# Optimization experiments

Hardware: AMD Instinct MI355X
Metric: run time of the kernel (lower is better)

## Reference

```python
import jax, jax.numpy as jnp
import numpy as np

B, S, D = 2, 2048, 1024
H, HD = 16, 64          # num_heads, head_dim
K = 32                  # JL n_components


def setup_inputs() -> dict:
    key = jax.random.key(0)
    k1, k2, k3, k4 = jax.random.split(key, 4)
    return {
        "hidden_states": jax.random.normal(k1, (B, S, D), dtype=jnp.float32),
        "W_attn": jax.random.normal(k2, (D, 3 * D), dtype=jnp.float32) * 0.02,
        "b_attn": jnp.zeros((3 * D,), dtype=jnp.float32),
        "S_proj": jax.random.normal(k3, (K, HD), dtype=jnp.float32) / np.sqrt(K),
        "W_proj": jax.random.normal(k4, (D, D), dtype=jnp.float32) * 0.02,
        "b_proj": jnp.zeros((D,), dtype=jnp.float32),
    }


def reference(hidden_states, W_attn, b_attn, S_proj, W_proj, b_proj):
    b, s, d = hidden_states.shape
    # GPT2 Conv1D: x @ W + b, then split into q,k,v
    qkv = hidden_states @ W_attn + b_attn            # [B,S,3D]
    q, k, v = jnp.split(qkv, 3, axis=-1)
    # split heads -> [B,H,S,HD]
    def split_heads(x):
        return x.reshape(b, s, H, HD).transpose(0, 2, 1, 3)
    q = split_heads(q) @ S_proj.T                    # [B,H,S,K] JL-reduced
    k = split_heads(k) @ S_proj.T                    # [B,H,S,K]
    v = split_heads(v)                               # [B,H,S,HD]
    # naive attention: scale by sqrt(value head_dim) per GPT2 _attn
    scores = jnp.einsum("bhqk,bhsk->bhqs", q, k) / jnp.sqrt(
        jnp.asarray(HD, dtype=v.dtype))              # [B,H,S,S]
    causal = jnp.tril(jnp.ones((s, s), dtype=bool))
    mask_value = jnp.finfo(scores.dtype).min
    scores = jnp.where(causal, scores, mask_value)
    attn = jax.nn.softmax(scores, axis=-1)
    out = jnp.einsum("bhqs,bhsd->bhqd", attn, v)     # [B,H,S,HD]
    out = out.transpose(0, 2, 1, 3).reshape(b, s, d)  # merge heads
    return out @ W_proj + b_proj
```

## Files before the change

kernel.cpp:

```cpp
#include <hip/hip_runtime.h>
#include <hip/hip_bf16.h>
#include <stdint.h>

#define B_ 2
#define S_ 2048
#define D_ 1024
#define H_ 16
#define HD_ 64
#define KJL 32
#define N3 3072

typedef __attribute__((ext_vector_type(8))) __bf16 bf16x8;
typedef __attribute__((ext_vector_type(4))) float floatx4;
typedef __attribute__((ext_vector_type(4))) short short4v;
typedef __attribute__((ext_vector_type(2))) unsigned int uint2v;

__device__ __forceinline__ unsigned short f2b(float x) {
  union { float f; unsigned u; } v; v.f = x;
  unsigned r = v.u + 0x7fffu + ((v.u >> 16) & 1u);
  return (unsigned short)(r >> 16);
}

__device__ __forceinline__ unsigned int pkbf(float lo, float hi) {
  union { float f; unsigned u; } a, b;
  a.f = lo; b.f = hi;
  return __builtin_amdgcn_perm(b.u + 0x8000u, a.u + 0x8000u, 0x07060302u);
}

__device__ __forceinline__ void async16(const void* g, void* l) {
  __builtin_amdgcn_global_load_lds((__attribute__((address_space(1))) void*)(g),
                                   (__attribute__((address_space(3))) void*)(l),
                                   16, 0, 0);
}

__global__ void cvt_kernel(const float* __restrict__ in,
                           unsigned short* __restrict__ out, int n) {
  int i = blockIdx.x * blockDim.x + threadIdx.x;
  int stride = gridDim.x * blockDim.x;
  for (; i < n; i += stride) out[i] = f2b(in[i]);
}

__global__ void tcvt_kernel(const float* __restrict__ in,
                            unsigned short* __restrict__ out, int R, int C) {
  __shared__ float t[32][33];
  int c0 = blockIdx.x * 32, r0 = blockIdx.y * 32;
  int tx = threadIdx.x, ty = threadIdx.y;
  for (int j = 0; j < 32; j += 8)
    t[ty + j][tx] = in[(r0 + ty + j) * C + c0 + tx];
  __syncthreads();
  for (int j = 0; j < 32; j += 8)
    out[(c0 + ty + j) * R + r0 + tx] = f2b(t[tx][ty + j]);
}

__global__ __launch_bounds__(256, 2)
void qkv_gemm_kernel(const unsigned short* __restrict__ A,
                     const unsigned short* __restrict__ Bt,
                     const float* __restrict__ bias,
                     unsigned short* __restrict__ Qh,
                     unsigned short* __restrict__ Kh,
                     unsigned short* __restrict__ Vc) {
  __shared__ __align__(16) unsigned short As[128 * 32];
  __shared__ __align__(16) unsigned short Bs[128 * 32];
  const int tid = threadIdx.x;
  const int lane = tid & 63, wv = tid >> 6;
  const int quad = lane >> 4, col = lane & 15;
  const int wm = wv >> 1, wn = wv & 1;
  const int m0 = blockIdx.y * 128, n0 = blockIdx.x * 128;

  floatx4 acc[4][4] = {};

  for (int kk = 0; kk < D_; kk += 32) {
    for (int it = 0; it < 2; ++it) {
      int c = it * 256 + tid;
      int row = c >> 2, k8 = (c & 3) << 3;
      async16(A + (m0 + row) * D_ + kk + k8, &As[c * 8]);
      async16(Bt + (n0 + row) * D_ + kk + k8, &Bs[c * 8]);
    }
    asm volatile("s_waitcnt vmcnt(0)" ::: "memory");
    __syncthreads();
    bf16x8 af[4], bfr[4];
    for (int mt = 0; mt < 4; ++mt)
      af[mt] = *(const bf16x8*)&As[(wm * 64 + mt * 16 + col) * 32 + quad * 8];
    for (int nt = 0; nt < 4; ++nt)
      bfr[nt] = *(const bf16x8*)&Bs[(wn * 64 + nt * 16 + col) * 32 + quad * 8];
    for (int mt = 0; mt < 4; ++mt)
      for (int nt = 0; nt < 4; ++nt)
        acc[mt][nt] = __builtin_amdgcn_mfma_f32_16x16x32_bf16(
            af[mt], bfr[nt], acc[mt][nt], 0, 0, 0);
    __syncthreads();
  }

  const int part = n0 >> 10;
  for (int mt = 0; mt < 4; ++mt) {
    int gm0 = m0 + wm * 64 + mt * 16 + quad * 4;
    int b = gm0 >> 11, s = gm0 & (S_ - 1);
    for (int nt = 0; nt < 4; ++nt) {
      int gn = n0 + wn * 64 + nt * 16 + col;
      float bs = bias[gn];
      int h = (gn >> 6) & (H_ - 1);
      int hd = gn & (HD_ - 1);
      if (part == 2) {
        short4v vv;
        for (int i = 0; i < 4; ++i)
          vv[i] = (short)f2b(acc[mt][nt][i] + bs);
        size_t idx = ((((size_t)(b * H_ + h) * 64 + (s >> 5)) * 64 + hd) * 32 + (s & 31));
        *(short4v*)&Vc[idx] = vv;
      } else {
        unsigned short* dst = (part == 0) ? Qh : Kh;
        int base = ((b * H_ + h) * S_ + s) * HD_ + hd;
        for (int i = 0; i < 4; ++i)
          dst[base + i * HD_] = f2b(acc[mt][nt][i] + bs);
      }
    }
  }
}

__global__ __launch_bounds__(256)
void jl_kernel(const unsigned short* __restrict__ X,
               const unsigned short* __restrict__ Sp,
               unsigned short* __restrict__ Y, float scale) {
  const int tid = threadIdx.x;
  const int lane = tid & 63, wv = tid >> 6;
  const int quad = lane >> 4, col = lane & 15;
  const int rowbase = blockIdx.x * 256 + wv * 64;
  bf16x8 bfr[2][2];
  for (int nt = 0; nt < 2; ++nt)
    for (int ks = 0; ks < 2; ++ks)
      bfr[nt][ks] = *(const bf16x8*)&Sp[(nt * 16 + col) * 64 + ks * 32 + quad * 8];
  for (int mt = 0; mt < 4; ++mt) {
    floatx4 acc[2] = {};
    for (int ks = 0; ks < 2; ++ks) {
      bf16x8 af = *(const bf16x8*)&X[(rowbase + mt * 16 + col) * 64 + ks * 32 + quad * 8];
      for (int nt = 0; nt < 2; ++nt)
        acc[nt] = __builtin_amdgcn_mfma_f32_16x16x32_bf16(af, bfr[nt][ks], acc[nt], 0, 0, 0);
    }
    for (int nt = 0; nt < 2; ++nt)
      for (int i = 0; i < 4; ++i)
        Y[(rowbase + mt * 16 + quad * 4 + i) * 32 + nt * 16 + col] =
            f2b(acc[nt][i] * scale);
  }
}

__global__ __launch_bounds__(256, 2)
void attn_kernel(const unsigned short* __restrict__ Qjl,
                 const unsigned short* __restrict__ Kjl,
                 const unsigned short* __restrict__ Vc,
                 unsigned short* __restrict__ AO) {
  __shared__ __align__(16) unsigned short Ps[4][32 * 136];
  const int tid = threadIdx.x;
  const int lane = tid & 63, wv = tid >> 6;
  const int quad = lane >> 4, l15 = lane & 15;

  const int blk = blockIdx.x;
  const int xcd = blk & 7;
  const int u = blk >> 3;
  const int bhl = (u >> 4) & 3;
  const int g0 = u & 15;
  const int g = (u & 32) ? (15 - g0) : g0;
  const int bh = xcd * 4 + bhl;
  const int t = 63 - (g * 4 + wv);
  const int b = bh >> 4, h = bh & 15;

  unsigned short* Pw = &Ps[wv][0];
  const int laneK = l15 * KJL + quad * 8;
  const int laneV = l15 * 32 + quad * 8;
  const unsigned short* Kp = Kjl + (size_t)bh * S_ * KJL + laneK;
  const unsigned short* Vp = Vc + (size_t)bh * (64 * 64 * 32) + laneV;

  bf16x8 aq[2];
  for (int qn = 0; qn < 2; ++qn)
    aq[qn] = *(const bf16x8*)&Qjl[(size_t)(bh * S_ + t * 32 + qn * 16 + l15) * KJL + quad * 8];

  floatx4 o[4][2] = {};
  floatx4 psum[2] = {};
  const floatx4 zz = {0.f, 0.f, 0.f, 0.f};

  const int lastc = t >> 2;
  const int r = t & 3;

  for (int kt = 0; kt <= lastc; ++kt) {
    bf16x8 ak[8];
    for (int sm = 0; sm < 8; ++sm)
      ak[sm] = *(const bf16x8*)&Kp[sm * (16 * KJL)];
    bf16x8 bv[4][4];
    for (int ks = 0; ks < 4; ++ks)
      for (int md = 0; md < 4; ++md)
        bv[ks][md] = *(const bf16x8*)&Vp[ks * 2048 + md * 512];
    Kp += 128 * KJL;
    Vp += 8192;

    floatx4 sc[8][2];
    for (int sm = 0; sm < 8; ++sm)
      for (int qn = 0; qn < 2; ++qn)
        sc[sm][qn] = __builtin_amdgcn_mfma_f32_16x16x32_bf16(ak[sm], aq[qn], zz, 0, 0, 0);

    if (kt == lastc) {
      for (int qn = 0; qn < 2; ++qn) {
        int qloc = r * 32 + qn * 16 + l15;
        for (int sm = 0; sm < 8; ++sm)
          for (int i = 0; i < 4; ++i)
            if (sm * 16 + quad * 4 + i > qloc) sc[sm][qn][i] = -1e30f;
      }
    }

    for (int qn = 0; qn < 2; ++qn) {
      for (int sm = 0; sm < 8; ++sm) {
        float p0 = __builtin_amdgcn_exp2f(sc[sm][qn][0]);
        float p1 = __builtin_amdgcn_exp2f(sc[sm][qn][1]);
        float p2 = __builtin_amdgcn_exp2f(sc[sm][qn][2]);
        float p3 = __builtin_amdgcn_exp2f(sc[sm][qn][3]);
        psum[qn][0] += p0; psum[qn][1] += p1;
        psum[qn][2] += p2; psum[qn][3] += p3;
        uint2v pk2 = {pkbf(p0, p1), pkbf(p2, p3)};
        *(uint2v*)&Pw[(qn * 16 + l15) * 136 + sm * 16 + quad * 4] = pk2;
      }
    }

    for (int ks = 0; ks < 4; ++ks) {
      bf16x8 bp[2];
      for (int qn = 0; qn < 2; ++qn)
        bp[qn] = *(const bf16x8*)&Pw[(qn * 16 + l15) * 136 + ks * 32 + quad * 8];
      for (int qn = 0; qn < 2; ++qn)
        for (int md = 0; md < 4; ++md)
          o[md][qn] = __builtin_amdgcn_mfma_f32_16x16x32_bf16(bv[ks][md], bp[qn], o[md][qn], 0, 0, 0);
    }
  }

  for (int qn = 0; qn < 2; ++qn) {
    float l = psum[qn][0] + psum[qn][1] + psum[qn][2] + psum[qn][3];
    l += __shfl_xor(l, 16, 64);
    l += __shfl_xor(l, 32, 64);
    float inv = 1.f / l;
    for (int md = 0; md < 4; ++md) {
      uint2v t4 = {pkbf(o[md][qn][0] * inv, o[md][qn][1] * inv),
                   pkbf(o[md][qn][2] * inv, o[md][qn][3] * inv)};
      *(uint2v*)&Pw[(qn * 16 + l15) * 72 + md * 16 + quad * 4] = t4;
    }
  }
  {
    int q = lane >> 1, half = lane & 1;
    size_t gbase = ((size_t)(b * S_ + t * 32 + q)) * D_ + h * HD_ + half * 32;
    for (int jj = 0; jj < 4; ++jj) {
      bf16x8 v = *(const bf16x8*)&Pw[q * 72 + half * 32 + jj * 8];
      *(bf16x8*)&AO[gbase + jj * 8] = v;
    }
  }
}

__global__ __launch_bounds__(256, 2)
void proj_gemm_kernel(const unsigned short* __restrict__ A,
                      const unsigned short* __restrict__ Bt,
                      const float* __restrict__ bias,
                      float* __restrict__ out) {
  __shared__ __align__(16) unsigned short As[128 * 32];
  __shared__ __align__(16) unsigned short Bs[128 * 32];
  const int tid = threadIdx.x;
  const int lane = tid & 63, wv = tid >> 6;
  const int quad = lane >> 4, col = lane & 15;
  const int wm = wv >> 1, wn = wv & 1;
  const int m0 = blockIdx.y * 128, n0 = blockIdx.x * 128;

  floatx4 acc[4][4] = {};

  for (int kk = 0; kk < D_; kk += 32) {
    for (int it = 0; it < 2; ++it) {
      int c = it * 256 + tid;
      int row = c >> 2, k8 = (c & 3) << 3;
      async16(A + (m0 + row) * D_ + kk + k8, &As[c * 8]);
      async16(Bt + (n0 + row) * D_ + kk + k8, &Bs[c * 8]);
    }
    asm volatile("s_waitcnt vmcnt(0)" ::: "memory");
    __syncthreads();
    bf16x8 af[4], bfr[4];
    for (int mt = 0; mt < 4; ++mt)
      af[mt] = *(const bf16x8*)&As[(wm * 64 + mt * 16 + col) * 32 + quad * 8];
    for (int nt = 0; nt < 4; ++nt)
      bfr[nt] = *(const bf16x8*)&Bs[(wn * 64 + nt * 16 + col) * 32 + quad * 8];
    for (int mt = 0; mt < 4; ++mt)
      for (int nt = 0; nt < 4; ++nt)
        acc[mt][nt] = __builtin_amdgcn_mfma_f32_16x16x32_bf16(
            af[mt], bfr[nt], acc[mt][nt], 0, 0, 0);
    __syncthreads();
  }

  for (int mt = 0; mt < 4; ++mt) {
    int gm0 = m0 + wm * 64 + mt * 16 + quad * 4;
    for (int nt = 0; nt < 4; ++nt) {
      int gn = n0 + wn * 64 + nt * 16 + col;
      float bs = bias[gn];
      for (int i = 0; i < 4; ++i)
        out[(gm0 + i) * D_ + gn] = acc[mt][nt][i] + bs;
    }
  }
}

extern "C" void kernel_launch(void* const* d_in, const int* in_sizes, int n_in,
                              void* d_out, int out_size, void* d_ws, size_t ws_size,
                              hipStream_t stream) {
  (void)in_sizes; (void)n_in; (void)out_size; (void)ws_size;
  const float* hidden = (const float*)d_in[0];
  const float* W_attn = (const float*)d_in[1];
  const float* b_attn = (const float*)d_in[2];
  const float* S_proj = (const float*)d_in[3];
  const float* W_proj = (const float*)d_in[4];
  const float* b_proj = (const float*)d_in[5];
  float* out = (float*)d_out;

  char* ws = (char*)d_ws;
  unsigned short* hB  = (unsigned short*)(ws);
  unsigned short* WaT = (unsigned short*)(ws + 8388608);
  unsigned short* WpT = (unsigned short*)(ws + 14680064);
  unsigned short* Qh  = (unsigned short*)(ws + 16777216);
  unsigned short* Kh  = (unsigned short*)(ws + 25165824);
  unsigned short* Vt  = (unsigned short*)(ws + 33554432);
  unsigned short* Qjl = (unsigned short*)(ws + 41943040);
  unsigned short* Kjl = (unsigned short*)(ws + 46137344);
  unsigned short* AO  = (unsigned short*)(ws + 50331648);
  unsigned short* Spb = (unsigned short*)(ws + 58720256);

  cvt_kernel<<<2048, 256, 0, stream>>>(hidden, hB, B_ * S_ * D_);
  cvt_kernel<<<8, 256, 0, stream>>>(S_proj, Spb, KJL * HD_);
  tcvt_kernel<<<dim3(N3 / 32, D_ / 32), dim3(32, 8), 0, stream>>>(W_attn, WaT, D_, N3);
  tcvt_kernel<<<dim3(D_ / 32, D_ / 32), dim3(32, 8), 0, stream>>>(W_proj, WpT, D_, D_);
  qkv_gemm_kernel<<<dim3(N3 / 128, (B_ * S_) / 128), 256, 0, stream>>>(
      hB, WaT, b_attn, Qh, Kh, Vt);
  jl_kernel<<<256, 256, 0, stream>>>(Qh, Spb, Qjl, 0.125f * 1.44269504f);
  jl_kernel<<<256, 256, 0, stream>>>(Kh, Spb, Kjl, 1.0f);
  attn_kernel<<<512, 256, 0, stream>>>(Qjl, Kjl, Vt, AO);
  proj_gemm_kernel<<<dim3(D_ / 128, (B_ * S_) / 128), 256, 0, stream>>>(
      AO, WpT, b_proj, out);
}
```

Baseline: 192.6 us.

## Fold JL projection into QKV weights and prefetch K tiles in attention

Precomputes W_q·S^T and W_k·S^T (with scale and projected bias) in a new weight-fold kernel, so the QKV GEMM produces JL-reduced Q and K directly with N=2048 instead of 3072. This removes the separate JL kernels and the full-width Q/K intermediate writes. It also vectorizes the input fp32→bf16 conversion and double-buffers the K fragment loads in the attention loop. The cost is an extra per-call weight-folding pass done in fp32 with poor parallelism (128 blocks, 64-float register arrays per thread). It also changes rounding, since the projection is now applied before bf16 quantization.

```diff
diff --git a/kernel.cpp b/kernel.cpp
--- a/kernel.cpp
+++ b/kernel.cpp
@@ -9,6 +9,7 @@
 #define HD_ 64
 #define KJL 32
 #define N3 3072
+#define N2 2048
 
 typedef __attribute__((ext_vector_type(8))) __bf16 bf16x8;
 typedef __attribute__((ext_vector_type(4))) float floatx4;
@@ -33,32 +34,70 @@
                                    16, 0, 0);
 }
 
-__global__ void cvt_kernel(const float* __restrict__ in,
-                           unsigned short* __restrict__ out, int n) {
+__global__ void cvt4_kernel(const float* __restrict__ in,
+                            unsigned short* __restrict__ out, int n4) {
   int i = blockIdx.x * blockDim.x + threadIdx.x;
   int stride = gridDim.x * blockDim.x;
-  for (; i < n; i += stride) out[i] = f2b(in[i]);
+  for (; i < n4; i += stride) {
+    float4 v = *(const float4*)(in + 4 * (size_t)i);
+    short4v o = {(short)f2b(v.x), (short)f2b(v.y), (short)f2b(v.z), (short)f2b(v.w)};
+    *(short4v*)(out + 4 * (size_t)i) = o;
+  }
 }
 
 __global__ void tcvt_kernel(const float* __restrict__ in,
-                            unsigned short* __restrict__ out, int R, int C) {
+                            unsigned short* __restrict__ out, int R, int Cs) {
   __shared__ float t[32][33];
   int c0 = blockIdx.x * 32, r0 = blockIdx.y * 32;
   int tx = threadIdx.x, ty = threadIdx.y;
   for (int j = 0; j < 32; j += 8)
-    t[ty + j][tx] = in[(r0 + ty + j) * C + c0 + tx];
+    t[ty + j][tx] = in[(size_t)(r0 + ty + j) * Cs + c0 + tx];
   __syncthreads();
   for (int j = 0; j < 32; j += 8)
-    out[(c0 + ty + j) * R + r0 + tx] = f2b(t[tx][ty + j]);
+    out[(size_t)(c0 + ty + j) * R + r0 + tx] = f2b(t[tx][ty + j]);
+}
+
+__global__ __launch_bounds__(256)
+void wjl_kernel(const float* __restrict__ W_attn, const float* __restrict__ b_attn,
+                const float* __restrict__ Sp, unsigned short* __restrict__ Bt2,
+                float* __restrict__ bias2) {
+  __shared__ float SpL[32 * 64];
+  const int bid = blockIdx.x;
+  const int part = bid >> 6;
+  const int h = (bid >> 2) & 15;
+  const int dc = bid & 3;
+  const int tid = threadIdx.x;
+  for (int i = tid; i < 32 * 64; i += 256) SpL[i] = Sp[i];
+  __syncthreads();
+  const float scale = part ? 1.0f : 0.125f * 1.44269504f;
+  const int d = dc * 256 + tid;
+  float w[64];
+  const float* src = W_attn + (size_t)d * N3 + part * D_ + h * 64;
+  for (int j = 0; j < 16; ++j) {
+    float4 v = *(const float4*)&src[j * 4];
+    w[j * 4 + 0] = v.x; w[j * 4 + 1] = v.y; w[j * 4 + 2] = v.z; w[j * 4 + 3] = v.w;
+  }
+  const int nbase = part * 512 + h * 32;
+  for (int kjl = 0; kjl < 32; ++kjl) {
+    float acc = 0.f;
+    for (int hd = 0; hd < 64; ++hd) acc += w[hd] * SpL[kjl * 64 + hd];
+    Bt2[(size_t)(nbase + kjl) * D_ + d] = f2b(acc * scale);
+  }
+  if (dc == 0 && tid < 32) {
+    float acc = 0.f;
+    for (int hd = 0; hd < 64; ++hd) acc += b_attn[part * D_ + h * 64 + hd] * SpL[tid * 64 + hd];
+    bias2[nbase + tid] = acc * scale;
+  }
 }
 
 __global__ __launch_bounds__(256, 2)
-void qkv_gemm_kernel(const unsigned short* __restrict__ A,
-                     const unsigned short* __restrict__ Bt,
-                     const float* __restrict__ bias,
-                     unsigned short* __restrict__ Qh,
-                     unsigned short* __restrict__ Kh,
-                     unsigned short* __restrict__ Vc) {
+void qkv2_gemm_kernel(const unsigned short* __restrict__ A,
+                      const unsigned short* __restrict__ Bt,
+                      const float* __restrict__ b_attn,
+                      const float* __restrict__ bias2,
+                      unsigned short* __restrict__ Qjl,
+                      unsigned short* __restrict__ Kjl,
+                      unsigned short* __restrict__ Vc) {
   __shared__ __align__(16) unsigned short As[128 * 32];
   __shared__ __align__(16) unsigned short Bs[128 * 32];
   const int tid = threadIdx.x;
@@ -73,8 +112,8 @@
     for (int it = 0; it < 2; ++it) {
       int c = it * 256 + tid;
       int row = c >> 2, k8 = (c & 3) << 3;
-      async16(A + (m0 + row) * D_ + kk + k8, &As[c * 8]);
-      async16(Bt + (n0 + row) * D_ + kk + k8, &Bs[c * 8]);
+      async16(A + (size_t)(m0 + row) * D_ + kk + k8, &As[c * 8]);
+      async16(Bt + (size_t)(n0 + row) * D_ + kk + k8, &Bs[c * 8]);
     }
     asm volatile("s_waitcnt vmcnt(0)" ::: "memory");
     __syncthreads();
@@ -90,54 +129,31 @@
     __syncthreads();
   }
 
-  const int part = n0 >> 10;
+  const int pq = n0 >> 9;
   for (int mt = 0; mt < 4; ++mt) {
     int gm0 = m0 + wm * 64 + mt * 16 + quad * 4;
     int b = gm0 >> 11, s = gm0 & (S_ - 1);
     for (int nt = 0; nt < 4; ++nt) {
       int gn = n0 + wn * 64 + nt * 16 + col;
-      float bs = bias[gn];
-      int h = (gn >> 6) & (H_ - 1);
-      int hd = gn & (HD_ - 1);
-      if (part == 2) {
+      if (pq >= 2) {
+        int vcol = gn - 1024;
+        float bs = b_attn[2048 + vcol];
+        int h = vcol >> 6, hd = vcol & 63;
         short4v vv;
         for (int i = 0; i < 4; ++i)
           vv[i] = (short)f2b(acc[mt][nt][i] + bs);
         size_t idx = ((((size_t)(b * H_ + h) * 64 + (s >> 5)) * 64 + hd) * 32 + (s & 31));
         *(short4v*)&Vc[idx] = vv;
       } else {
-        unsigned short* dst = (part == 0) ? Qh : Kh;
-        int base = ((b * H_ + h) * S_ + s) * HD_ + hd;
+        float bs = bias2[gn];
+        int gl = gn & 511;
+        int h = gl >> 5, kjl = gl & 31;
+        unsigned short* dst = pq ? Kjl : Qjl;
+        size_t base = ((size_t)(b * H_ + h) * S_ + s) * KJL + kjl;
         for (int i = 0; i < 4; ++i)
-          dst[base + i * HD_] = f2b(acc[mt][nt][i] + bs);
+          dst[base + (size_t)i * KJL] = f2b(acc[mt][nt][i] + bs);
       }
     }
-  }
-}
-
-__global__ __launch_bounds__(256)
-void jl_kernel(const unsigned short* __restrict__ X,
-               const unsigned short* __restrict__ Sp,
-               unsigned short* __restrict__ Y, float scale) {
-  const int tid = threadIdx.x;
-  const int lane = tid & 63, wv = tid >> 6;
-  const int quad = lane >> 4, col = lane & 15;
-  const int rowbase = blockIdx.x * 256 + wv * 64;
-  bf16x8 bfr[2][2];
-  for (int nt = 0; nt < 2; ++nt)
-    for (int ks = 0; ks < 2; ++ks)
-      bfr[nt][ks] = *(const bf16x8*)&Sp[(nt * 16 + col) * 64 + ks * 32 + quad * 8];
-  for (int mt = 0; mt < 4; ++mt) {
-    floatx4 acc[2] = {};
-    for (int ks = 0; ks < 2; ++ks) {
-      bf16x8 af = *(const bf16x8*)&X[(rowbase + mt * 16 + col) * 64 + ks * 32 + quad * 8];
-      for (int nt = 0; nt < 2; ++nt)
-        acc[nt] = __builtin_amdgcn_mfma_f32_16x16x32_bf16(af, bfr[nt][ks], acc[nt], 0, 0, 0);
-    }
-    for (int nt = 0; nt < 2; ++nt)
-      for (int i = 0; i < 4; ++i)
-        Y[(rowbase + mt * 16 + quad * 4 + i) * 32 + nt * 16 + col] =
-            f2b(acc[nt][i] * scale);
   }
 }
 
@@ -178,21 +194,28 @@
   const int lastc = t >> 2;
   const int r = t & 3;
 
+  bf16x8 akb[2][8];
+  for (int sm = 0; sm < 8; ++sm)
+    akb[0][sm] = *(const bf16x8*)&Kp[sm * (16 * KJL)];
+  Kp += 128 * KJL;
+
   for (int kt = 0; kt <= lastc; ++kt) {
-    bf16x8 ak[8];
-    for (int sm = 0; sm < 8; ++sm)
-      ak[sm] = *(const bf16x8*)&Kp[sm * (16 * KJL)];
+    const int cur = kt & 1;
     bf16x8 bv[4][4];
     for (int ks = 0; ks < 4; ++ks)
       for (int md = 0; md < 4; ++md)
         bv[ks][md] = *(const bf16x8*)&Vp[ks * 2048 + md * 512];
-    Kp += 128 * KJL;
     Vp += 8192;
+    if (kt < lastc) {
+      for (int sm = 0; sm < 8; ++sm)
+        akb[cur ^ 1][sm] = *(const bf16x8*)&Kp[sm * (16 * KJL)];
+      Kp += 128 * KJL;
+    }
 
     floatx4 sc[8][2];
     for (int sm = 0; sm < 8; ++sm)
       for (int qn = 0; qn < 2; ++qn)
-        sc[sm][qn] = __builtin_amdgcn_mfma_f32_16x16x32_bf16(ak[sm], aq[qn], zz, 0, 0, 0);
+        sc[sm][qn] = __builtin_amdgcn_mfma_f32_16x16x32_bf16(akb[cur][sm], aq[qn], zz, 0, 0, 0);
 
     if (kt == lastc) {
       for (int qn = 0; qn < 2; ++qn) {
@@ -266,8 +289,8 @@
     for (int it = 0; it < 2; ++it) {
       int c = it * 256 + tid;
       int row = c >> 2, k8 = (c & 3) << 3;
-      async16(A + (m0 + row) * D_ + kk + k8, &As[c * 8]);
-      async16(Bt + (n0 + row) * D_ + kk + k8, &Bs[c * 8]);
+      async16(A + (size_t)(m0 + row) * D_ + kk + k8, &As[c * 8]);
+      async16(Bt + (size_t)(n0 + row) * D_ + kk + k8, &Bs[c * 8]);
     }
     asm volatile("s_waitcnt vmcnt(0)" ::: "memory");
     __syncthreads();
@@ -289,7 +312,7 @@
       int gn = n0 + wn * 64 + nt * 16 + col;
       float bs = bias[gn];
       for (int i = 0; i < 4; ++i)
-        out[(gm0 + i) * D_ + gn] = acc[mt][nt][i] + bs;
+        out[(size_t)(gm0 + i) * D_ + gn] = acc[mt][nt][i] + bs;
     }
   }
 }
@@ -307,26 +330,22 @@
   float* out = (float*)d_out;
 
   char* ws = (char*)d_ws;
-  unsigned short* hB  = (unsigned short*)(ws);
-  unsigned short* WaT = (unsigned short*)(ws + 8388608);
-  unsigned short* WpT = (unsigned short*)(ws + 14680064);
-  unsigned short* Qh  = (unsigned short*)(ws + 16777216);
-  unsigned short* Kh  = (unsigned short*)(ws + 25165824);
-  unsigned short* Vt  = (unsigned short*)(ws + 33554432);
-  unsigned short* Qjl = (unsigned short*)(ws + 41943040);
-  unsigned short* Kjl = (unsigned short*)(ws + 46137344);
-  unsigned short* AO  = (unsigned short*)(ws + 50331648);
-  unsigned short* Spb = (unsigned short*)(ws + 58720256);
-
-  cvt_kernel<<<2048, 256, 0, stream>>>(hidden, hB, B_ * S_ * D_);
-  cvt_kernel<<<8, 256, 0, stream>>>(S_proj, Spb, KJL * HD_);
-  tcvt_kernel<<<dim3(N3 / 32, D_ / 32), dim3(32, 8), 0, stream>>>(W_attn, WaT, D_, N3);
-  tcvt_kernel<<<dim3(D_ / 32, D_ / 32), dim3(32, 8), 0, stream>>>(W_proj, WpT, D_, D_);
-  qkv_gemm_kernel<<<dim3(N3 / 128, (B_ * S_) / 128), 256, 0, stream>>>(
-      hB, WaT, b_attn, Qh, Kh, Vt);
-  jl_kernel<<<256, 256, 0, stream>>>(Qh, Spb, Qjl, 0.125f * 1.44269504f);
-  jl_kernel<<<256, 256, 0, stream>>>(Kh, Spb, Kjl, 1.0f);
-  attn_kernel<<<512, 256, 0, stream>>>(Qjl, Kjl, Vt, AO);
+  unsigned short* hB    = (unsigned short*)(ws);
+  unsigned short* Bt2   = (unsigned short*)(ws + (8u << 20));
+  unsigned short* WpT   = (unsigned short*)(ws + (12u << 20));
+  float*          bias2 = (float*)         (ws + (14u << 20));
+  unsigned short* Qjl   = (unsigned short*)(ws + (15u << 20));
+  unsigned short* Kjl   = (unsigned short*)(ws + (19u << 20));
+  unsigned short* Vc    = (unsigned short*)(ws + (23u << 20));
+  unsigned short* AO    = (unsigned short*)(ws + (31u << 20));
+
+  cvt4_kernel<<<2048, 256, 0, stream>>>(hidden, hB, (B_ * S_ * D_) / 4);
+  tcvt_kernel<<<dim3(32, 32), dim3(32, 8), 0, stream>>>(W_attn + 2048, Bt2 + 1024 * 1024, D_, N3);
+  tcvt_kernel<<<dim3(32, 32), dim3(32, 8), 0, stream>>>(W_proj, WpT, D_, D_);
+  wjl_kernel<<<128, 256, 0, stream>>>(W_attn, b_attn, S_proj, Bt2, bias2);
+  qkv2_gemm_kernel<<<dim3(N2 / 128, (B_ * S_) / 128), 256, 0, stream>>>(
+      hB, Bt2, b_attn, bias2, Qjl, Kjl, Vc);
+  attn_kernel<<<512, 256, 0, stream>>>(Qjl, Kjl, Vc, AO);
   proj_gemm_kernel<<<dim3(D_ / 128, (B_ * S_) / 128), 256, 0, stream>>>(
       AO, WpT, b_proj, out);
 }
```

New measurement: 220.9 us. +14.7%, slower.
